# Performance work log

Hardware: AMD Instinct MI355X
Metric: run time of the kernel (lower is better)

Reference implementation:

```python
import jax, jax.numpy as jnp
import numpy as np

LATENT = 512
RNN = 512
CODE = 512
INP = 2
MIX = 5
BATCH = 4096
SEGMENTS = 512


def _p(key, shape, scale=0.05):
    return jax.random.normal(key, shape, dtype=jnp.float32) * scale


def setup_inputs() -> dict:
    key = jax.random.key(0)
    ks = jax.random.split(key, 20)
    return {
        "latent": jax.random.normal(ks[0], (BATCH, LATENT), dtype=jnp.float32),
        "W_unpack": _p(ks[1], (CODE, LATENT)),
        "b_unpack": _p(ks[2], (CODE,)),
        "W_ih1": _p(ks[3], (4 * RNN, CODE + INP)),
        "W_hh1": _p(ks[4], (4 * RNN, RNN)),
        "b_ih1": _p(ks[5], (4 * RNN,)),
        "b_hh1": _p(ks[6], (4 * RNN,)),
        "W_ih2": _p(ks[7], (4 * RNN, RNN)),
        "W_hh2": _p(ks[8], (4 * RNN, RNN)),
        "b_ih2": _p(ks[9], (4 * RNN,)),
        "b_hh2": _p(ks[10], (4 * RNN,)),
        "W_mu": _p(ks[11], (MIX, RNN)),
        "b_mu": _p(ks[12], (MIX,)),
        "W_var": _p(ks[13], (MIX, RNN)),
        "b_var": _p(ks[14], (MIX,)),
        "W_mix": _p(ks[15], (MIX, RNN)),
        "b_mix": _p(ks[16], (MIX,)),
        "eps": jax.random.normal(ks[17], (SEGMENTS, BATCH, 1), dtype=jnp.float32),
        "num_segments": SEGMENTS,
    }


def _lstm_cell(x, h, c, W_ih, W_hh, b_ih, b_hh):
    # PyTorch LSTMCell: gate order i, f, g, o
    gates = x @ W_ih.T + b_ih + h @ W_hh.T + b_hh
    i, f, g, o = jnp.split(gates, 4, axis=-1)
    c_new = jax.nn.sigmoid(f) * c + jax.nn.sigmoid(i) * jnp.tanh(g)
    h_new = jax.nn.sigmoid(o) * jnp.tanh(c_new)
    return h_new, c_new


def reference(latent, W_unpack, b_unpack, W_ih1, W_hh1, b_ih1, b_hh1,
              W_ih2, W_hh2, b_ih2, b_hh2, W_mu, b_mu, W_var, b_var,
              W_mix, b_mix, eps, num_segments):
    t = 0.0  # default temperature arg
    B = latent.shape[0]
    idea = jnp.tanh(latent @ W_unpack.T + b_unpack)  # [B, CODE]

    def step(carry, eps_s):
        prev, h1, c1, h2, c2 = carry
        x = jnp.concatenate([idea, prev], axis=-1)          # [B, CODE+2]
        h1, c1 = _lstm_cell(x, h1, c1, W_ih1, W_hh1, b_ih1, b_hh1)
        h2, c2 = _lstm_cell(h1, h2, c2, W_ih2, W_hh2, b_ih2, b_hh2)
        rho = jax.nn.softmax(h2 @ W_mix.T + b_mix, axis=-1)  # [B, MIX]
        mu = jnp.sum(rho * (h2 @ W_mu.T + b_mu), axis=-1, keepdims=True)
        sigma = jnp.sum(rho * jnp.exp(h2 @ W_var.T + b_var - t), axis=-1, keepdims=True)
        angles = jnp.tanh(mu + sigma * eps_s)                # rsample + tanh, [B, 1]
        prev = jnp.concatenate([angles, jnp.zeros_like(angles)], axis=-1)
        return (prev, h1, c1, h2, c2), angles

    z = jnp.zeros((B, RNN), dtype=latent.dtype)
    carry0 = (jnp.zeros((B, INP), dtype=latent.dtype), z, z, z, z)
    _, angles = jax.lax.scan(step, carry0, eps)              # [S, B, 1]
    level = jnp.concatenate([angles, jnp.zeros_like(angles)], axis=-1)  # [S, B, 2]
    return jnp.transpose(level, (1, 0, 2))                   # [B, S, 2]
```

## Files before the change

kernel.cpp:

```cpp
#include <hip/hip_runtime.h>
#include <stdint.h>

#define BATCH 4096
#define RNN   512
#define SEGS  512

typedef __attribute__((ext_vector_type(8))) short bf16x8;
typedef __attribute__((ext_vector_type(4))) float f32x4;

#define MODE_TANH  0
#define MODE_BASE  1
#define MODE_CELL1 2
#define MODE_CELL2 3

__device__ __forceinline__ unsigned short f2bf(float f){
  unsigned u = __float_as_uint(f);
  u += 0x7FFF + ((u >> 16) & 1);
  return (unsigned short)(u >> 16);
}
__device__ __forceinline__ float bf2f(unsigned short s){
  return __uint_as_float(((unsigned)s) << 16);
}
__device__ __forceinline__ float fsigmoid(float x){ return 1.0f / (1.0f + __expf(-x)); }
__device__ __forceinline__ float ftanh(float x){
  float e = __expf(-2.0f * fabsf(x));
  float t = (1.0f - e) / (1.0f + e);
  return copysignf(t, x);
}


__global__ void prep_cvt(const float* __restrict__ x, short* __restrict__ y, int n){
  int i = blockIdx.x * 256 + threadIdx.x;
  if (i < n) y[i] = (short)f2bf(x[i]);
}

__global__ void prep_reorder(
    const float* __restrict__ W_ih1, const float* __restrict__ W_hh1,
    const float* __restrict__ b_ih1, const float* __restrict__ b_hh1,
    const float* __restrict__ W_ih2, const float* __restrict__ W_hh2,
    const float* __restrict__ b_ih2, const float* __restrict__ b_hh2,
    short* __restrict__ Wr1, short* __restrict__ W1c,
    short* __restrict__ Wr2i, short* __restrict__ Wr2h,
    float* __restrict__ w1r, float* __restrict__ b1r, float* __restrict__ b2r)
{
  int idx = blockIdx.x * 256 + threadIdx.x;
  if (idx >= 2048 * 512) return;
  int rn = idx >> 9;
  int k  = idx & 511;
  int j = rn >> 2, g = rn & 3;
  int ro = g * 512 + j;
  Wr1 [idx] = (short)f2bf(W_hh1[(size_t)ro * 512 + k]);
  W1c [idx] = (short)f2bf(W_ih1[(size_t)ro * 514 + k]);
  Wr2i[idx] = (short)f2bf(W_ih2[(size_t)ro * 512 + k]);
  Wr2h[idx] = (short)f2bf(W_hh2[(size_t)ro * 512 + k]);
  if (k == 0){
    w1r[rn] = W_ih1[(size_t)ro * 514 + 512];
    b1r[rn] = b_ih1[ro] + b_hh1[ro];
    b2r[rn] = b_ih2[ro] + b_hh2[ro];
  }
}

__global__ __launch_bounds__(256) void gemm_fused(
    const short* __restrict__ A1, const short* __restrict__ B1,
    const short* __restrict__ A2, const short* __restrict__ B2,
    int k1, int k2, int N, int mode,
    const float* __restrict__ bias,
    const float* __restrict__ base1,
    const float* __restrict__ w1r,
    const float* __restrict__ ang,
    float* __restrict__ cbuf,
    void* __restrict__ outp)
{
  __shared__ __align__(16) short As[128 * 72];
  __shared__ __align__(16) short Bs[128 * 72];
  const int tid  = threadIdx.x;
  const int lane = tid & 63;
  const int wave = tid >> 6;
  const int wm = wave >> 1, wn = wave & 1;
  const int m0 = blockIdx.y * 128, n0 = blockIdx.x * 128;

  f32x4 acc[4][4];
  #pragma unroll
  for (int i = 0; i < 4; i++)
    #pragma unroll
    for (int j = 0; j < 4; j++)
      acc[i][j] = (f32x4){0.f, 0.f, 0.f, 0.f};

  const int nk = (k1 + k2) >> 6;
  for (int it = 0; it < nk; ++it){
    int ko = it << 6;
    const short* Ap; const short* Bp; int kk;
    if (ko < k1){ Ap = A1; Bp = B1; kk = ko; }
    else        { Ap = A2; Bp = B2; kk = ko - k1; }
    #pragma unroll
    for (int i = 0; i < 4; i++){
      int c = i * 256 + tid;
      int row = c >> 3, c8 = (c & 7) << 3;
      *(uint4*)&As[row * 72 + c8] = *(const uint4*)&Ap[(size_t)(m0 + row) * 512 + kk + c8];
      *(uint4*)&Bs[row * 72 + c8] = *(const uint4*)&Bp[(size_t)(n0 + row) * 512 + kk + c8];
    }
    __syncthreads();
    #pragma unroll
    for (int kw = 0; kw < 2; ++kw){
      bf16x8 af[4], bfr[4];
      const int ro = (lane & 15) * 72 + kw * 32 + (lane >> 4) * 8;
      #pragma unroll
      for (int f = 0; f < 4; f++){
        af[f]  = *(const bf16x8*)&As[(wm * 64 + f * 16) * 72 + ro];
        bfr[f] = *(const bf16x8*)&Bs[(wn * 64 + f * 16) * 72 + ro];
      }
      #pragma unroll
      for (int mf = 0; mf < 4; mf++)
        #pragma unroll
        for (int nf = 0; nf < 4; nf++)
          acc[mf][nf] = __builtin_amdgcn_mfma_f32_16x16x32_bf16(af[mf], bfr[nf], acc[mf][nf], 0, 0, 0);
    }
    __syncthreads();
  }

  const int lr = (lane >> 4) * 4;
  const int lc = lane & 15;

  if (mode == MODE_TANH){
    unsigned short* out = (unsigned short*)outp;
    #pragma unroll
    for (int mf = 0; mf < 4; mf++)
      #pragma unroll
      for (int nf = 0; nf < 4; nf++)
        #pragma unroll
        for (int r = 0; r < 4; r++){
          int grow = m0 + wm * 64 + mf * 16 + lr + r;
          int gcol = n0 + wn * 64 + nf * 16 + lc;
          float v = acc[mf][nf][r] + bias[gcol];
          out[(size_t)grow * N + gcol] = f2bf(ftanh(v));
        }
  } else if (mode == MODE_BASE){
    float* out = (float*)outp;
    #pragma unroll
    for (int mf = 0; mf < 4; mf++)
      #pragma unroll
      for (int nf = 0; nf < 4; nf++)
        #pragma unroll
        for (int r = 0; r < 4; r++){
          int grow = m0 + wm * 64 + mf * 16 + lr + r;
          int gcol = n0 + wn * 64 + nf * 16 + lc;
          out[(size_t)grow * N + gcol] = acc[mf][nf][r] + bias[gcol];
        }
  } else {
    unsigned short* hout = (unsigned short*)outp;
    const int q = lane & 3;
    #pragma unroll
    for (int mf = 0; mf < 4; mf++)
      #pragma unroll
      for (int nf = 0; nf < 4; nf++)
        #pragma unroll
        for (int r = 0; r < 4; r++){
          int grow = m0 + wm * 64 + mf * 16 + lr + r;
          int gcol = n0 + wn * 64 + nf * 16 + lc;
          float v = acc[mf][nf][r];
          if (mode == MODE_CELL1)
            v += base1[(size_t)grow * 2048 + gcol] + ang[grow] * w1r[gcol];
          else
            v += bias[gcol];
          float x1 = __shfl_xor(v, 1);
          float x2 = __shfl_xor(v, 2);
          float x3 = __shfl_xor(v, 3);
          if (q == 0){
            int j = gcol >> 2;
            size_t ci = (size_t)grow * 512 + j;
            float co = cbuf[ci];
            float cn = fsigmoid(x1) * co + fsigmoid(v) * ftanh(x2);
            float hn = fsigmoid(x3) * ftanh(cn);
            cbuf[ci] = cn;
            hout[ci] = f2bf(hn);
          }
        }
  }
}

__global__ __launch_bounds__(256) void head_step(
    const short* __restrict__ h2,
    const float* __restrict__ Wmu,  const float* __restrict__ bmu,
    const float* __restrict__ Wvar, const float* __restrict__ bvar,
    const float* __restrict__ Wmix, const float* __restrict__ bmix,
    const float* __restrict__ eps,  float* __restrict__ ang,
    float* __restrict__ out, int s)
{
  const int lane = threadIdx.x & 63;
  const int wave = threadIdx.x >> 6;
  const int row = blockIdx.x * 4 + wave;

  uint4 hv = *(const uint4*)&h2[(size_t)row * 512 + lane * 8];
  const unsigned short* hs = (const unsigned short*)&hv;
  float h[8];
  #pragma unroll
  for (int j = 0; j < 8; j++) h[j] = bf2f(hs[j]);

  float p[15];
  #pragma unroll
  for (int k = 0; k < 5; k++){
    const float4* wm4 = (const float4*)(Wmu  + (size_t)k * 512 + lane * 8);
    const float4* wv4 = (const float4*)(Wvar + (size_t)k * 512 + lane * 8);
    const float4* wx4 = (const float4*)(Wmix + (size_t)k * 512 + lane * 8);
    float4 a0 = wm4[0], a1 = wm4[1];
    float4 v0 = wv4[0], v1 = wv4[1];
    float4 x0 = wx4[0], x1 = wx4[1];
    p[k]      = h[0]*a0.x + h[1]*a0.y + h[2]*a0.z + h[3]*a0.w + h[4]*a1.x + h[5]*a1.y + h[6]*a1.z + h[7]*a1.w;
    p[5 + k]  = h[0]*v0.x + h[1]*v0.y + h[2]*v0.z + h[3]*v0.w + h[4]*v1.x + h[5]*v1.y + h[6]*v1.z + h[7]*v1.w;
    p[10 + k] = h[0]*x0.x + h[1]*x0.y + h[2]*x0.z + h[3]*x0.w + h[4]*x1.x + h[5]*x1.y + h[6]*x1.z + h[7]*x1.w;
  }
  #pragma unroll
  for (int k = 0; k < 15; k++){
    #pragma unroll
    for (int off = 1; off < 64; off <<= 1)
      p[k] += __shfl_xor(p[k], off);
  }
  if (lane == 0){
    float l[5], mx = -1e30f;
    #pragma unroll
    for (int k = 0; k < 5; k++){ l[k] = p[10 + k] + bmix[k]; mx = fmaxf(mx, l[k]); }
    float se = 0.f, e[5];
    #pragma unroll
    for (int k = 0; k < 5; k++){ e[k] = __expf(l[k] - mx); se += e[k]; }
    float inv = 1.0f / se, mu = 0.f, sg = 0.f;
    #pragma unroll
    for (int k = 0; k < 5; k++){
      float rho = e[k] * inv;
      mu += rho * (p[k] + bmu[k]);
      sg += rho * __expf(p[5 + k] + bvar[k]);
    }
    float a = ftanh(mu + sg * eps[(size_t)s * BATCH + row]);
    ang[row] = a;
    size_t o = ((size_t)row * SEGS + s) * 2;
    out[o]     = a;
    out[o + 1] = 0.0f;
  }
}


extern "C" void kernel_launch(void* const* d_in, const int* in_sizes, int n_in,
                              void* d_out, int out_size, void* d_ws, size_t ws_size,
                              hipStream_t stream)
{
  const float* latent   = (const float*)d_in[0];
  const float* W_unpack = (const float*)d_in[1];
  const float* b_unpack = (const float*)d_in[2];
  const float* W_ih1    = (const float*)d_in[3];
  const float* W_hh1    = (const float*)d_in[4];
  const float* b_ih1    = (const float*)d_in[5];
  const float* b_hh1    = (const float*)d_in[6];
  const float* W_ih2    = (const float*)d_in[7];
  const float* W_hh2    = (const float*)d_in[8];
  const float* b_ih2    = (const float*)d_in[9];
  const float* b_hh2    = (const float*)d_in[10];
  const float* W_mu     = (const float*)d_in[11];
  const float* b_mu     = (const float*)d_in[12];
  const float* W_var    = (const float*)d_in[13];
  const float* b_var    = (const float*)d_in[14];
  const float* W_mix    = (const float*)d_in[15];
  const float* b_mix    = (const float*)d_in[16];
  const float* eps      = (const float*)d_in[17];
  float* out = (float*)d_out;

  char* p = (char*)d_ws;
  auto alloc = [&](size_t b) -> void* {
    void* r = (void*)p;
    p += (b + 255) & ~(size_t)255;
    return r;
  };
  short* latb  = (short*)alloc((size_t)BATCH * 512 * 2);
  short* Wub   = (short*)alloc((size_t)512 * 512 * 2);
  short* idea  = (short*)alloc((size_t)BATCH * 512 * 2);
  float* base1 = (float*)alloc((size_t)BATCH * 2048 * 4);
  short* Wr1   = (short*)alloc((size_t)2048 * 512 * 2);
  short* W1c   = (short*)alloc((size_t)2048 * 512 * 2);
  short* Wr2i  = (short*)alloc((size_t)2048 * 512 * 2);
  short* Wr2h  = (short*)alloc((size_t)2048 * 512 * 2);
  float* w1r   = (float*)alloc(2048 * 4);
  float* b1r   = (float*)alloc(2048 * 4);
  float* b2r   = (float*)alloc(2048 * 4);
  short* h1a   = (short*)alloc((size_t)BATCH * 512 * 2);
  short* h1b   = (short*)alloc((size_t)BATCH * 512 * 2);
  short* h2a   = (short*)alloc((size_t)BATCH * 512 * 2);
  short* h2b   = (short*)alloc((size_t)BATCH * 512 * 2);
  float* c1    = (float*)alloc((size_t)BATCH * 512 * 4);
  float* c2    = (float*)alloc((size_t)BATCH * 512 * 4);
  float* ang   = (float*)alloc(BATCH * 4);
  short* h1[2] = {h1a, h1b};
  short* h2[2] = {h2a, h2b};

  hipMemsetAsync(h1[0], 0, (size_t)BATCH * 512 * 2, stream);
  hipMemsetAsync(h2[0], 0, (size_t)BATCH * 512 * 2, stream);
  hipMemsetAsync(c1, 0, (size_t)BATCH * 512 * 4, stream);
  hipMemsetAsync(c2, 0, (size_t)BATCH * 512 * 4, stream);
  hipMemsetAsync(ang, 0, BATCH * 4, stream);

  prep_cvt<<<(BATCH * 512) / 256, 256, 0, stream>>>(latent, latb, BATCH * 512);
  prep_cvt<<<(512 * 512) / 256, 256, 0, stream>>>(W_unpack, Wub, 512 * 512);
  prep_reorder<<<(2048 * 512) / 256, 256, 0, stream>>>(
      W_ih1, W_hh1, b_ih1, b_hh1, W_ih2, W_hh2, b_ih2, b_hh2,
      Wr1, W1c, Wr2i, Wr2h, w1r, b1r, b2r);

  dim3 blk(256);
  gemm_fused<<<dim3(512 / 128, 32), blk, 0, stream>>>(
      latb, Wub, nullptr, nullptr, 512, 0, 512, MODE_TANH,
      b_unpack, nullptr, nullptr, nullptr, nullptr, (void*)idea);
  gemm_fused<<<dim3(2048 / 128, 32), blk, 0, stream>>>(
      idea, W1c, nullptr, nullptr, 512, 0, 2048, MODE_BASE,
      b1r, nullptr, nullptr, nullptr, nullptr, (void*)base1);

  int cur = 0;
  for (int s = 0; s < SEGS; ++s){
    gemm_fused<<<dim3(16, 32), blk, 0, stream>>>(
        h1[cur], Wr1, nullptr, nullptr, 512, 0, 2048, MODE_CELL1,
        nullptr, base1, w1r, ang, c1, (void*)h1[cur ^ 1]);
    gemm_fused<<<dim3(16, 32), blk, 0, stream>>>(
        h1[cur ^ 1], Wr2i, h2[cur], Wr2h, 512, 512, 2048, MODE_CELL2,
        b2r, nullptr, nullptr, nullptr, c2, (void*)h2[cur ^ 1]);
    head_step<<<BATCH / 4, 256, 0, stream>>>(
        h2[cur ^ 1], W_mu, b_mu, W_var, b_var, W_mix, b_mix, eps, ang, out, s);
    cur ^= 1;
  }
}
```

Baseline: 63.81 ms.

## Fuse mixture head into LSTM cell1 GEMM and use direct global-to-LDS loads

The per-step head kernel is removed. Each cell1 block now recomputes, with MFMA, the head projections for its 128 rows from the previous h2, then derives the sampled angle into shared memory and writes the output once from block column 0. Operand tiles are loaded with global_load_lds into a fragment-ordered LDS layout instead of a padded register copy. base1 is stored in bf16 to halve its traffic. This cuts a launch and a sync per step, at the cost of redundant head work in all 16 column blocks and some precision loss in base1.

```diff
diff --git a/kernel.cpp b/kernel.cpp
--- a/kernel.cpp
+++ b/kernel.cpp
@@ -12,6 +12,10 @@
 #define MODE_BASE  1
 #define MODE_CELL1 2
 #define MODE_CELL2 3
+
+#define GLD_LDS16(g, l) \
+  __builtin_amdgcn_global_load_lds((const __attribute__((address_space(1))) void*)(g), \
+                                   (__attribute__((address_space(3))) void*)(l), 16, 0, 0)
 
 __device__ __forceinline__ unsigned short f2bf(float f){
   unsigned u = __float_as_uint(f);
@@ -60,25 +64,51 @@
   }
 }
 
+__global__ void prep_whead(const float* __restrict__ Wmu, const float* __restrict__ Wvar,
+                           const float* __restrict__ Wmix, short* __restrict__ Wh){
+  int i = blockIdx.x * 256 + threadIdx.x;
+  if (i >= 16 * 512) return;
+  int n = i >> 9, k = i & 511;
+  float v = (n < 5) ? Wmu[n * 512 + k] : (n < 10) ? Wvar[(n - 5) * 512 + k]
+          : (n < 15) ? Wmix[(n - 10) * 512 + k] : 0.f;
+  Wh[i] = (short)f2bf(v);
+}
+
 __global__ __launch_bounds__(256) void gemm_fused(
     const short* __restrict__ A1, const short* __restrict__ B1,
     const short* __restrict__ A2, const short* __restrict__ B2,
     int k1, int k2, int N, int mode,
     const float* __restrict__ bias,
-    const float* __restrict__ base1,
+    const unsigned short* __restrict__ base1,
     const float* __restrict__ w1r,
-    const float* __restrict__ ang,
     float* __restrict__ cbuf,
-    void* __restrict__ outp)
+    void* __restrict__ outp,
+    const short* __restrict__ h2prev, const short* __restrict__ Whead,
+    const float* __restrict__ bmu, const float* __restrict__ bvar,
+    const float* __restrict__ bmix, const float* __restrict__ eps,
+    float* __restrict__ fout, int s)
 {
-  __shared__ __align__(16) short As[128 * 72];
-  __shared__ __align__(16) short Bs[128 * 72];
+  __shared__ __align__(16) short As[8192];
+  __shared__ __align__(16) short Bs[8192];
+  __shared__ __align__(16) float headP[128 * 16];
+  __shared__ float angS[128];
+
   const int tid  = threadIdx.x;
   const int lane = tid & 63;
   const int wave = tid >> 6;
   const int wm = wave >> 1, wn = wave & 1;
   const int m0 = blockIdx.y * 128, n0 = blockIdx.x * 128;
 
+  int aoff[4], boff[4];
+  #pragma unroll
+  for (int j = 0; j < 4; j++){
+    int c = (wave * 4 + j) * 64 + lane;
+    int quad = c & 3, r16 = (c >> 2) & 15, kw = (c >> 6) & 1, g = c >> 7;
+    int row = g * 16 + r16, col = kw * 32 + quad * 8;
+    aoff[j] = (m0 + row) * 512 + col;
+    boff[j] = (n0 + row) * 512 + col;
+  }
+
   f32x4 acc[4][4];
   #pragma unroll
   for (int i = 0; i < 4; i++)
@@ -87,27 +117,29 @@
       acc[i][j] = (f32x4){0.f, 0.f, 0.f, 0.f};
 
   const int nk = (k1 + k2) >> 6;
-  for (int it = 0; it < nk; ++it){
+
+  auto stage = [&](int it){
     int ko = it << 6;
     const short* Ap; const short* Bp; int kk;
     if (ko < k1){ Ap = A1; Bp = B1; kk = ko; }
     else        { Ap = A2; Bp = B2; kk = ko - k1; }
     #pragma unroll
-    for (int i = 0; i < 4; i++){
-      int c = i * 256 + tid;
-      int row = c >> 3, c8 = (c & 7) << 3;
-      *(uint4*)&As[row * 72 + c8] = *(const uint4*)&Ap[(size_t)(m0 + row) * 512 + kk + c8];
-      *(uint4*)&Bs[row * 72 + c8] = *(const uint4*)&Bp[(size_t)(n0 + row) * 512 + kk + c8];
+    for (int j = 0; j < 4; j++){
+      GLD_LDS16(Ap + aoff[j] + kk, (char*)As + (wave * 4 + j) * 1024);
+      GLD_LDS16(Bp + boff[j] + kk, (char*)Bs + (wave * 4 + j) * 1024);
     }
-    __syncthreads();
+  };
+
+  const int fro = ((lane & 15) * 4 + (lane >> 4)) * 8;
+
+  auto compute = [&](){
     #pragma unroll
     for (int kw = 0; kw < 2; ++kw){
       bf16x8 af[4], bfr[4];
-      const int ro = (lane & 15) * 72 + kw * 32 + (lane >> 4) * 8;
       #pragma unroll
       for (int f = 0; f < 4; f++){
-        af[f]  = *(const bf16x8*)&As[(wm * 64 + f * 16) * 72 + ro];
-        bfr[f] = *(const bf16x8*)&Bs[(wn * 64 + f * 16) * 72 + ro];
+        af[f]  = *(const bf16x8*)&As[((wm * 4 + f) * 2 + kw) * 512 + fro];
+        bfr[f] = *(const bf16x8*)&Bs[((wn * 4 + f) * 2 + kw) * 512 + fro];
       }
       #pragma unroll
       for (int mf = 0; mf < 4; mf++)
@@ -115,6 +147,68 @@
         for (int nf = 0; nf < 4; nf++)
           acc[mf][nf] = __builtin_amdgcn_mfma_f32_16x16x32_bf16(af[mf], bfr[nf], acc[mf][nf], 0, 0, 0);
     }
+  };
+
+  stage(0);
+
+  if (mode == MODE_CELL1 && s > 0){
+    const int g0 = wave * 2;
+    f32x4 pa0 = {0.f,0.f,0.f,0.f}, pa1 = {0.f,0.f,0.f,0.f};
+    const int arow = m0 + g0 * 16 + (lane & 15);
+    const int koff = (lane >> 4) * 8;
+    #pragma unroll
+    for (int k0 = 0; k0 < 512; k0 += 32){
+      bf16x8 bfh = *(const bf16x8*)&Whead[(lane & 15) * 512 + k0 + koff];
+      bf16x8 a0  = *(const bf16x8*)&h2prev[(size_t)arow * 512 + k0 + koff];
+      bf16x8 a1  = *(const bf16x8*)&h2prev[(size_t)(arow + 16) * 512 + k0 + koff];
+      pa0 = __builtin_amdgcn_mfma_f32_16x16x32_bf16(a0, bfh, pa0, 0, 0, 0);
+      pa1 = __builtin_amdgcn_mfma_f32_16x16x32_bf16(a1, bfh, pa1, 0, 0, 0);
+    }
+    #pragma unroll
+    for (int r = 0; r < 4; r++){
+      headP[((g0    ) * 16 + (lane >> 4) * 4 + r) * 16 + (lane & 15)] = pa0[r];
+      headP[((g0 + 1) * 16 + (lane >> 4) * 4 + r) * 16 + (lane & 15)] = pa1[r];
+    }
+  }
+
+  __syncthreads();
+
+  if (mode == MODE_CELL1){
+    if (s > 0){
+      if (tid < 128){
+        float p[15];
+        #pragma unroll
+        for (int k = 0; k < 15; k++) p[k] = headP[tid * 16 + k];
+        float l[5], mx = -1e30f;
+        #pragma unroll
+        for (int k = 0; k < 5; k++){ l[k] = p[10 + k] + bmix[k]; mx = fmaxf(mx, l[k]); }
+        float se = 0.f, e[5];
+        #pragma unroll
+        for (int k = 0; k < 5; k++){ e[k] = __expf(l[k] - mx); se += e[k]; }
+        float inv = 1.0f / se, mu = 0.f, sg = 0.f;
+        #pragma unroll
+        for (int k = 0; k < 5; k++){
+          float rho = e[k] * inv;
+          mu += rho * (p[k] + bmu[k]);
+          sg += rho * __expf(p[5 + k] + bvar[k]);
+        }
+        float a = ftanh(mu + sg * eps[(size_t)(s - 1) * BATCH + m0 + tid]);
+        angS[tid] = a;
+        if (blockIdx.x == 0){
+          size_t o = ((size_t)(m0 + tid) * SEGS + (s - 1)) * 2;
+          fout[o] = a; fout[o + 1] = 0.0f;
+        }
+      }
+    } else if (tid < 128) angS[tid] = 0.f;
+  }
+
+  compute();
+  __syncthreads();
+
+  for (int it = 1; it < nk; ++it){
+    stage(it);
+    __syncthreads();
+    compute();
     __syncthreads();
   }
 
@@ -135,7 +229,7 @@
           out[(size_t)grow * N + gcol] = f2bf(ftanh(v));
         }
   } else if (mode == MODE_BASE){
-    float* out = (float*)outp;
+    unsigned short* out = (unsigned short*)outp;
     #pragma unroll
     for (int mf = 0; mf < 4; mf++)
       #pragma unroll
@@ -144,7 +238,7 @@
         for (int r = 0; r < 4; r++){
           int grow = m0 + wm * 64 + mf * 16 + lr + r;
           int gcol = n0 + wn * 64 + nf * 16 + lc;
-          out[(size_t)grow * N + gcol] = acc[mf][nf][r] + bias[gcol];
+          out[(size_t)grow * N + gcol] = f2bf(acc[mf][nf][r] + bias[gcol]);
         }
   } else {
     unsigned short* hout = (unsigned short*)outp;
@@ -159,7 +253,7 @@
           int gcol = n0 + wn * 64 + nf * 16 + lc;
           float v = acc[mf][nf][r];
           if (mode == MODE_CELL1)
-            v += base1[(size_t)grow * 2048 + gcol] + ang[grow] * w1r[gcol];
+            v += bf2f(base1[(size_t)grow * 2048 + gcol]) + angS[grow - m0] * w1r[gcol];
           else
             v += bias[gcol];
           float x1 = __shfl_xor(v, 1);
@@ -271,11 +365,12 @@
   short* latb  = (short*)alloc((size_t)BATCH * 512 * 2);
   short* Wub   = (short*)alloc((size_t)512 * 512 * 2);
   short* idea  = (short*)alloc((size_t)BATCH * 512 * 2);
-  float* base1 = (float*)alloc((size_t)BATCH * 2048 * 4);
+  unsigned short* base1 = (unsigned short*)alloc((size_t)BATCH * 2048 * 2);
   short* Wr1   = (short*)alloc((size_t)2048 * 512 * 2);
   short* W1c   = (short*)alloc((size_t)2048 * 512 * 2);
   short* Wr2i  = (short*)alloc((size_t)2048 * 512 * 2);
   short* Wr2h  = (short*)alloc((size_t)2048 * 512 * 2);
+  short* Whead = (short*)alloc((size_t)16 * 512 * 2);
   float* w1r   = (float*)alloc(2048 * 4);
   float* b1r   = (float*)alloc(2048 * 4);
   float* b2r   = (float*)alloc(2048 * 4);
@@ -293,32 +388,36 @@
   hipMemsetAsync(h2[0], 0, (size_t)BATCH * 512 * 2, stream);
   hipMemsetAsync(c1, 0, (size_t)BATCH * 512 * 4, stream);
   hipMemsetAsync(c2, 0, (size_t)BATCH * 512 * 4, stream);
-  hipMemsetAsync(ang, 0, BATCH * 4, stream);
 
   prep_cvt<<<(BATCH * 512) / 256, 256, 0, stream>>>(latent, latb, BATCH * 512);
   prep_cvt<<<(512 * 512) / 256, 256, 0, stream>>>(W_unpack, Wub, 512 * 512);
   prep_reorder<<<(2048 * 512) / 256, 256, 0, stream>>>(
       W_ih1, W_hh1, b_ih1, b_hh1, W_ih2, W_hh2, b_ih2, b_hh2,
       Wr1, W1c, Wr2i, Wr2h, w1r, b1r, b2r);
+  prep_whead<<<32, 256, 0, stream>>>(W_mu, W_var, W_mix, Whead);
 
   dim3 blk(256);
-  gemm_fused<<<dim3(512 / 128, 32), blk, 0, stream>>>(
+  gemm_fused<<<dim3(4, 32), blk, 0, stream>>>(
       latb, Wub, nullptr, nullptr, 512, 0, 512, MODE_TANH,
-      b_unpack, nullptr, nullptr, nullptr, nullptr, (void*)idea);
-  gemm_fused<<<dim3(2048 / 128, 32), blk, 0, stream>>>(
+      b_unpack, nullptr, nullptr, nullptr, (void*)idea,
+      nullptr, nullptr, nullptr, nullptr, nullptr, nullptr, nullptr, 0);
+  gemm_fused<<<dim3(16, 32), blk, 0, stream>>>(
       idea, W1c, nullptr, nullptr, 512, 0, 2048, MODE_BASE,
-      b1r, nullptr, nullptr, nullptr, nullptr, (void*)base1);
+      b1r, nullptr, nullptr, nullptr, (void*)base1,
+      nullptr, nullptr, nullptr, nullptr, nullptr, nullptr, nullptr, 0);
 
   int cur = 0;
   for (int s = 0; s < SEGS; ++s){
     gemm_fused<<<dim3(16, 32), blk, 0, stream>>>(
         h1[cur], Wr1, nullptr, nullptr, 512, 0, 2048, MODE_CELL1,
-        nullptr, base1, w1r, ang, c1, (void*)h1[cur ^ 1]);
+        nullptr, base1, w1r, c1, (void*)h1[cur ^ 1],
+        h2[cur], Whead, b_mu, b_var, b_mix, eps, out, s);
     gemm_fused<<<dim3(16, 32), blk, 0, stream>>>(
         h1[cur ^ 1], Wr2i, h2[cur], Wr2h, 512, 512, 2048, MODE_CELL2,
-        b2r, nullptr, nullptr, nullptr, c2, (void*)h2[cur ^ 1]);
-    head_step<<<BATCH / 4, 256, 0, stream>>>(
-        h2[cur ^ 1], W_mu, b_mu, W_var, b_var, W_mix, b_mix, eps, ang, out, s);
+        b2r, nullptr, nullptr, c2, (void*)h2[cur ^ 1],
+        nullptr, nullptr, nullptr, nullptr, nullptr, nullptr, nullptr, 0);
     cur ^= 1;
   }
-}
+  head_step<<<BATCH / 4, 256, 0, stream>>>(
+      h2[cur], W_mu, b_mu, W_var, b_var, W_mix, b_mix, eps, ang, out, SEGS - 1);
+}
```

Measured after the change: 61.07 ms. 1.04x faster.
